# Performance work log

Measured on AMD Instinct MI355X. Metric: run time of the kernel, lower is better.

## Reference

```python
import jax, jax.numpy as jnp
import numpy as np

EPS = 1e-5

def _conv1x1(x, w, b):
    # x: [B,C,H,W], w: [O,C], b: [O] -> [B,O,H,W]
    return jnp.einsum('bchw,oc->bohw', x, w) + b[None, :, None, None]

def setup_inputs() -> dict:
    key = jax.random.key(0)
    ks = jax.random.split(key, 13)
    B, C, H, W = 16, 256, 64, 64
    Ci = C // 2
    s = 0.05
    return {
        'x': jax.random.normal(ks[0], (B, C, H, W), jnp.float32),
        'g_w': jax.random.normal(ks[1], (Ci, C), jnp.float32) * s,
        'g_b': jax.random.normal(ks[2], (Ci,), jnp.float32) * s,
        'theta_w': jax.random.normal(ks[3], (Ci, C), jnp.float32) * s,
        'theta_b': jax.random.normal(ks[4], (Ci,), jnp.float32) * s,
        'phi_w': jax.random.normal(ks[5], (Ci, C), jnp.float32) * s,
        'phi_b': jax.random.normal(ks[6], (Ci,), jnp.float32) * s,
        'w_w': jax.random.normal(ks[7], (C, Ci), jnp.float32) * s,
        'w_b': jax.random.normal(ks[8], (C,), jnp.float32) * s,
        'bn_gamma': jax.random.normal(ks[9], (C,), jnp.float32),
        'bn_beta': jax.random.normal(ks[10], (C,), jnp.float32),
        'bn_mean': jax.random.normal(ks[11], (C,), jnp.float32),
        'bn_var': jax.random.uniform(ks[12], (C,), jnp.float32, 0.5, 1.5),
    }

def reference(x, g_w, g_b, theta_w, theta_b, phi_w, phi_b,
              w_w, w_b, bn_gamma, bn_beta, bn_mean, bn_var):
    B, C, H, W = x.shape
    N = H * W
    Ci = g_w.shape[0]
    # 1x1 conv projections, flatten spatial to N
    g_x = _conv1x1(x, g_w, g_b).reshape(B, Ci, N).transpose(0, 2, 1)        # [B,N,Ci]
    theta_x = _conv1x1(x, theta_w, theta_b).reshape(B, Ci, N).transpose(0, 2, 1)  # [B,N,Ci]
    phi_x = _conv1x1(x, phi_w, phi_b).reshape(B, Ci, N)                     # [B,Ci,N]
    # affinity f = theta @ phi, normalized by N (softmax-free linear attention)
    f_div_C = jnp.einsum('bnc,bcm->bnm', theta_x, phi_x) / N                # [B,N,N]
    y = jnp.einsum('bnm,bmc->bnc', f_div_C, g_x)                            # [B,N,Ci]
    y = y.transpose(0, 2, 1).reshape(B, Ci, H, W)
    # W: 1x1 conv + BatchNorm (eval mode, running stats)
    w_y = _conv1x1(y, w_w, w_b)
    inv = bn_gamma * jax.lax.rsqrt(bn_var + EPS)
    w_y = w_y * inv[None, :, None, None] + (bn_beta - bn_mean * inv)[None, :, None, None]
    return w_y + x
```

## Files before the change

### kernel.cpp

```cpp
#include <hip/hip_runtime.h>
#include <stdint.h>

#define BATCH 16
#define CH    256
#define CI    128
#define NSP   4096
#define KC    4
#define EPSV  1e-5f

typedef unsigned short u16;
typedef __attribute__((ext_vector_type(4))) float f32x4;
typedef __attribute__((ext_vector_type(8))) short bf16x8;

__device__ __forceinline__ u16 f2b(float f) {
  uint32_t u = __float_as_uint(f);
  uint32_t r = u + 0x7FFFu + ((u >> 16) & 1u);
  return (u16)(r >> 16);
}

__device__ __forceinline__ void async16(void* lds, const void* g) {
  __builtin_amdgcn_global_load_lds(
      (const __attribute__((address_space(1))) unsigned int*)g,
      (__attribute__((address_space(3))) unsigned int*)lds, 16, 0, 0);
}

__global__ __launch_bounds__(256) void k_prep2(const float* __restrict__ x,
    u16* __restrict__ xb, float* __restrict__ psum,
    const float* __restrict__ w_w, const float* __restrict__ g_w,
    const float* __restrict__ g_b, const float* __restrict__ theta_w,
    const float* __restrict__ theta_b, const float* __restrict__ phi_w,
    const float* __restrict__ phi_b, const float* __restrict__ w_b,
    const float* __restrict__ bn_g, const float* __restrict__ bn_b,
    const float* __restrict__ bn_m, const float* __restrict__ bn_v,
    float* __restrict__ E, float* __restrict__ KT, float* __restrict__ wg,
    float* __restrict__ tphi, float* __restrict__ q, float* __restrict__ inv,
    float* __restrict__ dconst, float* __restrict__ tb) {
  __shared__ float lbuf[1024];
  const int t = threadIdx.x;
  if (blockIdx.z == BATCH) {
    const int id = blockIdx.y*64 + blockIdx.x;
    if (id < 32) {
      const int o0 = id*8;
      #pragma unroll
      for (int k = 0; k < 4; ++k) { int idx = k*256 + t;
        lbuf[idx] = w_w[(size_t)(o0 + (idx & 7))*CI + (idx >> 3)]; }
      __syncthreads();
      float acc[8] = {0.f};
      for (int j = 0; j < CI; ++j) {
        float gv = g_w[(size_t)j*CH + t];
        #pragma unroll
        for (int r = 0; r < 8; ++r) acc[r] += lbuf[j*8 + r] * gv;
      }
      #pragma unroll
      for (int r = 0; r < 8; ++r) E[(size_t)(o0 + r)*CH + t] = acc[r];
    } else if (id < 64) {
      const int a0 = (id - 32)*8;
      #pragma unroll
      for (int k = 0; k < 4; ++k) { int idx = k*256 + t;
        lbuf[idx] = phi_w[(size_t)(idx >> 3)*CH + a0 + (idx & 7)]; }
      __syncthreads();
      float acc[8] = {0.f};
      for (int i = 0; i < CI; ++i) {
        float tv = theta_w[(size_t)i*CH + t];
        #pragma unroll
        for (int u = 0; u < 8; ++u) acc[u] += lbuf[i*8 + u] * tv;
      }
      #pragma unroll
      for (int u = 0; u < 8; ++u) KT[(size_t)(a0 + u)*CH + t] = acc[u];
    } else if (id == 64) {
      float iv = bn_g[t] * rsqrtf(bn_v[t] + EPSV);
      inv[t] = iv;
      dconst[t] = iv*w_b[t] + bn_b[t] - bn_m[t]*iv;
      float a = 0.f;
      for (int j = 0; j < CI; ++j) a += w_w[(size_t)t*CI + j] * g_b[j];
      wg[t] = a;
      float tp = 0.f, qq = 0.f;
      for (int i = 0; i < CI; ++i) {
        tp += theta_w[(size_t)i*CH + t] * phi_b[i];
        qq += phi_w[(size_t)i*CH + t] * theta_b[i];
      }
      tphi[t] = tp; q[t] = qq;
      lbuf[t] = (t < CI) ? theta_b[t]*phi_b[t] : 0.f;
      __syncthreads();
      for (int s2 = 128; s2 > 0; s2 >>= 1) { if (t < s2) lbuf[t] += lbuf[t + s2]; __syncthreads(); }
      if (t == 0) tb[0] = lbuf[0];
    }
    return;
  }
  const int b = blockIdx.z, c0 = blockIdx.y*64, n0 = blockIdx.x*64;
  const int lane8 = t & 7, rq = t >> 3;
  const float* xp = x + ((size_t)b*CH + c0)*NSP + n0 + lane8*8;
  u16* xbp = xb + ((size_t)b*CH + c0)*NSP + n0 + lane8*8;
  #pragma unroll
  for (int p = 0; p < 2; ++p) {
    const int cl = rq + p*32;
    float4 v0 = *(const float4*)(xp + (size_t)cl*NSP);
    float4 v1 = *(const float4*)(xp + (size_t)cl*NSP + 4);
    float ps = v0.x+v0.y+v0.z+v0.w + v1.x+v1.y+v1.z+v1.w;
    #pragma unroll
    for (int o = 1; o < 8; o <<= 1) ps += __shfl_xor(ps, o, 64);
    if (lane8 == 0) psum[((size_t)b*64 + blockIdx.x)*CH + c0 + cl] = ps;
    bf16x8 bv;
    bv[0]=(short)f2b(v0.x); bv[1]=(short)f2b(v0.y); bv[2]=(short)f2b(v0.z); bv[3]=(short)f2b(v0.w);
    bv[4]=(short)f2b(v1.x); bv[5]=(short)f2b(v1.y); bv[6]=(short)f2b(v1.z); bv[7]=(short)f2b(v1.w);
    *(bf16x8*)(xbp + (size_t)cl*NSP) = bv;
  }
}

__global__ __launch_bounds__(256) void k_tr(const u16* __restrict__ xb, u16* __restrict__ xt) {
  __shared__ u16 tl[64*256];
  const int b = blockIdx.y, n0 = blockIdx.x*64;
  const int t = threadIdx.x;
  const int lane8 = t & 7, rq = t >> 3;
  const u16* src = xb + (size_t)b*CH*NSP + n0;
  #pragma unroll
  for (int p = 0; p < 8; ++p) {
    const int c = rq + p*32;
    bf16x8 v = *(const bf16x8*)(src + (size_t)c*NSP + lane8*8);
    const int cs = c ^ (lane8 << 3);
    #pragma unroll
    for (int j = 0; j < 8; ++j)
      tl[(lane8*8 + j)*256 + cs] = (u16)v[j];
  }
  __syncthreads();
  const int c8 = t & 31, nl = t >> 5;
  u16* dst = xt + ((size_t)b*NSP + n0)*CH;
  #pragma unroll
  for (int p2 = 0; p2 < 8; ++p2) {
    const int n = p2*8 + nl;
    bf16x8 v = *(const bf16x8*)(tl + n*256 + ((c8*8) ^ (p2 << 3)));
    *(bf16x8*)(dst + (size_t)n*CH + c8*8) = v;
  }
}

__global__ __launch_bounds__(256) void k_gram(const u16* __restrict__ xb, float* __restrict__ Sp) {
  __shared__ u16 As[64*64];
  __shared__ u16 Bs[64*64];
  const int TIa[10] = {0,0,0,0,1,1,1,2,2,3};
  const int TJa[10] = {0,1,2,3,1,2,3,2,3,3};
  const int L = blockIdx.x;
  const int wk = (L & 7) * 80 + (L >> 3);
  const int b = wk / 40;
  const int rem = wk % 40;
  const int kc = rem / 10;
  const int tile = rem % 10;
  const int ti = TIa[tile], tj = TJa[tile];
  const int m_base = ti*64, n_base = tj*64;
  const bool diag = (ti == tj);
  const int t = threadIdx.x, wv = t >> 6, l = t & 63;
  const int wr = wv >> 1, wc = wv & 1;
  const int lr = l & 15, lkb = l >> 4;
  const int sr8 = l >> 3, ss = l & 7;
  const u16* xa = xb + (size_t)b*CH*NSP;
  const int kbeg = kc * (NSP/KC);
  f32x4 acc[2][2];
  #pragma unroll
  for (int i = 0; i < 2; ++i)
    #pragma unroll
    for (int j = 0; j < 2; ++j) acc[i][j] = (f32x4){0.f,0.f,0.f,0.f};

  for (int kk = 0; kk < 16; ++kk) {
    const int kpos = kbeg + kk*64;
    #pragma unroll
    for (int j = 0; j < 2; ++j) {
      const int g = wv*2 + j;
      const int r = g*8 + sr8;
      async16(&As[g*512], xa + (size_t)(m_base + r)*NSP + kpos + ((ss ^ (r & 7)) * 8));
    }
    if (!diag) {
      #pragma unroll
      for (int j = 0; j < 2; ++j) {
        const int g = wv*2 + j;
        const int r = g*8 + sr8;
        async16(&Bs[g*512], xa + (size_t)(n_base + r)*NSP + kpos + ((ss ^ (r & 7)) * 8));
      }
    }
    __syncthreads();
    const u16* bsrc = diag ? As : Bs;
    #pragma unroll
    for (int ks = 0; ks < 2; ++ks) {
      bf16x8 A[2], Bf[2];
      #pragma unroll
      for (int mt = 0; mt < 2; ++mt) {
        const int ra = wr*32 + mt*16 + lr;
        A[mt] = *(const bf16x8*)(As + ra*64 + (((ks*4 + lkb) ^ (ra & 7)) * 8));
      }
      #pragma unroll
      for (int nt = 0; nt < 2; ++nt) {
        const int rb = wc*32 + nt*16 + lr;
        Bf[nt] = *(const bf16x8*)(bsrc + rb*64 + (((ks*4 + lkb) ^ (rb & 7)) * 8));
      }
      #pragma unroll
      for (int mt = 0; mt < 2; ++mt)
        #pragma unroll
        for (int nt = 0; nt < 2; ++nt)
          acc[mt][nt] = __builtin_amdgcn_mfma_f32_16x16x32_bf16(A[mt], Bf[nt], acc[mt][nt], 0, 0, 0);
    }
    __syncthreads();
  }
  float* Sb = Sp + (size_t)((b*KC + kc)*10 + tile)*4096;
  const int r0 = (l >> 4) * 4;
  #pragma unroll
  for (int mt = 0; mt < 2; ++mt)
    #pragma unroll
    for (int nt = 0; nt < 2; ++nt)
      #pragma unroll
      for (int rr = 0; rr < 4; ++rr) {
        const int lm = wr*32 + mt*16 + r0 + rr;
        const int lc = wc*32 + nt*16 + lr;
        Sb[lm*64 + lc] = acc[mt][nt][rr];
      }
}

__global__ __launch_bounds__(256) void k_redvec(const float* __restrict__ Sp,
    const float* __restrict__ psum, const float* __restrict__ E,
    const float* __restrict__ KT, const float* __restrict__ q,
    float* __restrict__ S, float* __restrict__ KS, float* __restrict__ Es,
    float* __restrict__ qs) {
  __shared__ float tl[64*65 + 8];
  const int b = blockIdx.y, xx = blockIdx.x, t = threadIdx.x;
  if (xx < 10) {
    const int TIa[10] = {0,0,0,0,1,1,1,2,2,3};
    const int TJa[10] = {0,1,2,3,1,2,3,2,3,3};
    const int ti = TIa[xx], tj = TJa[xx];
    const int row0 = ti*64, col0 = tj*64;
    float* Sb = S + (size_t)b*CH*CH;
    float4 sum[4];
    #pragma unroll
    for (int k = 0; k < 4; ++k) {
      const int slot = t + k*256;
      const int r = slot >> 4, c4 = (slot & 15) * 4;
      float4 s = {0.f,0.f,0.f,0.f};
      #pragma unroll
      for (int kc = 0; kc < KC; ++kc) {
        const float* p = Sp + (size_t)((b*KC + kc)*10 + xx)*4096;
        float4 v = *(const float4*)(p + r*64 + c4);
        s.x += v.x; s.y += v.y; s.z += v.z; s.w += v.w;
      }
      sum[k] = s;
      *(float4*)(Sb + (size_t)(row0 + r)*CH + col0 + c4) = s;
    }
    if (ti != tj) {
      #pragma unroll
      for (int k = 0; k < 4; ++k) {
        const int slot = t + k*256;
        const int r = slot >> 4, c4 = (slot & 15) * 4;
        tl[r*65 + c4+0] = sum[k].x; tl[r*65 + c4+1] = sum[k].y;
        tl[r*65 + c4+2] = sum[k].z; tl[r*65 + c4+3] = sum[k].w;
      }
      __syncthreads();
      #pragma unroll
      for (int k = 0; k < 4; ++k) {
        const int slot = t + k*256;
        const int r = slot >> 4, c4 = (slot & 15) * 4;
        float4 v = { tl[(c4+0)*65 + r], tl[(c4+1)*65 + r],
                     tl[(c4+2)*65 + r], tl[(c4+3)*65 + r] };
        *(float4*)(Sb + (size_t)(col0 + r)*CH + row0 + c4) = v;
      }
    }
  } else {
    float s = 0.f;
    for (int nb = 0; nb < 64; ++nb) s += psum[((size_t)b*64 + nb)*CH + t];
    tl[t] = s;
    __syncthreads();
    float ks = 0.f;
    for (int a = 0; a < CH; ++a) ks += KT[(size_t)a*CH + t] * tl[a];
    KS[(size_t)b*CH + t] = ks;
    float es = 0.f;
    for (int c = 0; c < CH; ++c) es += E[(size_t)t*CH + c] * tl[c];
    Es[(size_t)b*CH + t] = es;
    float p = q[t] * tl[t];
    #pragma unroll
    for (int o = 1; o < 64; o <<= 1) p += __shfl_xor(p, o, 64);
    if ((t & 63) == 0) tl[4160 + (t >> 6)] = p;
    __syncthreads();
    if (t == 0) qs[b] = tl[4160] + tl[4161] + tl[4162] + tl[4163];
  }
}

__global__ __launch_bounds__(256) void k_RP(const float* __restrict__ S,
    const float* __restrict__ E, const float* __restrict__ KT,
    const float* __restrict__ q, const float* __restrict__ KS,
    const float* __restrict__ Es, const float* __restrict__ qs,
    const float* __restrict__ wg, const float* __restrict__ tphi,
    const float* __restrict__ inv, const float* __restrict__ dconst,
    const float* __restrict__ tb, u16* __restrict__ Pb, float* __restrict__ dv) {
  __shared__ float lEt[2048];
  __shared__ float lRt[2048];
  __shared__ float red[32];
  const int b = blockIdx.y, o0 = blockIdx.x*8, t = threadIdx.x;
  #pragma unroll
  for (int k = 0; k < 8; ++k) { int idx = k*256 + t;
    lEt[idx] = E[(size_t)(o0 + (idx & 7))*CH + (idx >> 3)]; }
  __syncthreads();
  const float* Sb = S + (size_t)b*CH*CH;
  float acc[8] = {0.f};
  for (int c = 0; c < CH; ++c) {
    float sv = Sb[(size_t)c*CH + t];
    #pragma unroll
    for (int r = 0; r < 8; ++r) acc[r] += lEt[c*8 + r] * sv;
  }
  #pragma unroll
  for (int r = 0; r < 8; ++r) lRt[t*8 + r] = acc[r];
  const float qt = q[t];
  #pragma unroll
  for (int r = 0; r < 8; ++r) {
    float p = acc[r] * qt;
    #pragma unroll
    for (int o = 1; o < 64; o <<= 1) p += __shfl_xor(p, o, 64);
    if ((t & 63) == 0) red[r*4 + (t >> 6)] = p;
  }
  __syncthreads();
  float acc2[8] = {0.f};
  for (int a = 0; a < CH; ++a) {
    float kv = KT[(size_t)a*CH + t];
    #pragma unroll
    for (int r = 0; r < 8; ++r) acc2[r] += lRt[a*8 + r] * kv;
  }
  const float ksv = KS[(size_t)b*CH + t], tpv = tphi[t];
  u16* Pbb = Pb + (size_t)b*CH*CH;
  #pragma unroll
  for (int r = 0; r < 8; ++r) {
    int o = o0 + r;
    float val = (acc2[r] + wg[o]*ksv + (Es[(size_t)b*CH + o] + (float)NSP*wg[o])*tpv)
                * inv[o] * (1.f/(float)NSP);
    if (o == t) val += 1.f;
    Pbb[(size_t)o*CH + t] = f2b(val);
  }
  if (t < 8) {
    int o = o0 + t;
    float iv = inv[o], wgo = wg[o], tb0 = tb[0];
    float rq = red[t*4] + red[t*4+1] + red[t*4+2] + red[t*4+3];
    float t2 = rq + wgo*qs[b] + Es[(size_t)b*CH + o]*tb0;
    dv[(size_t)b*CH + o] = iv*(t2*(1.f/(float)NSP) + wgo*tb0) + dconst[o];
  }
}

__global__ __launch_bounds__(512, 4) void k_apply(const u16* __restrict__ Pb,
    const u16* __restrict__ xt, const float* __restrict__ dv,
    float* __restrict__ out) {
  __shared__ union {
    u16   bx[64*256];
    float fe[8][16][68];
  } sm;
  const int b = blockIdx.y, n0 = blockIdx.x*64;
  const int t = threadIdx.x, w = t >> 6, l = t & 63;
  {
    const u16* src = xt + ((size_t)b*NSP + n0)*CH;
    const int r = t >> 3, sbase = t & 7;
    #pragma unroll
    for (int it = 0; it < 4; ++it) {
      int slot = sbase + it*8;
      bf16x8 v = *(const bf16x8*)(src + (size_t)r*CH + slot*8);
      *(bf16x8*)(sm.bx + r*256 + ((slot ^ (r & 7)) * 8)) = v;
    }
  }
  __syncthreads();
  const int m0 = w*32;
  const int lr = l & 15, lkb = l >> 4;
  const int sw = lr & 7;
  const u16* Pp = Pb + (size_t)b*CH*CH;
  f32x4 acc[2][4];
  #pragma unroll
  for (int i = 0; i < 2; ++i)
    #pragma unroll
    for (int j = 0; j < 4; ++j) acc[i][j] = (f32x4){0.f,0.f,0.f,0.f};
  #pragma unroll
  for (int kk = 0; kk < 8; ++kk) {
    bf16x8 A[2], Bf[4];
    #pragma unroll
    for (int mt = 0; mt < 2; ++mt)
      A[mt] = *(const bf16x8*)(Pp + (size_t)(m0 + mt*16 + lr)*CH + kk*32 + lkb*8);
    #pragma unroll
    for (int nt = 0; nt < 4; ++nt) {
      int slot = kk*4 + lkb;
      Bf[nt] = *(const bf16x8*)(sm.bx + (nt*16 + lr)*256 + ((slot ^ sw) * 8));
    }
    #pragma unroll
    for (int mt = 0; mt < 2; ++mt)
      #pragma unroll
      for (int nt = 0; nt < 4; ++nt)
        acc[mt][nt] = __builtin_amdgcn_mfma_f32_16x16x32_bf16(A[mt], Bf[nt], acc[mt][nt], 0, 0, 0);
  }
  __syncthreads();
  float* ob = out + (size_t)b*CH*NSP;
  const int r0 = (l >> 4) * 4;
  #pragma unroll
  for (int mt = 0; mt < 2; ++mt) {
    #pragma unroll
    for (int rr = 0; rr < 4; ++rr) {
      float dval = dv[(size_t)b*CH + m0 + mt*16 + r0 + rr];
      #pragma unroll
      for (int nt = 0; nt < 4; ++nt)
        sm.fe[w][r0 + rr][nt*16 + lr] = acc[mt][nt][rr] + dval;
    }
    #pragma unroll
    for (int i = 0; i < 4; ++i) {
      int s = l + 64*i;
      int rrow = s >> 4, c4 = (s & 15) * 4;
      float4 v = *(const float4*)&sm.fe[w][rrow][c4];
      *(float4*)&ob[(size_t)(m0 + mt*16 + rrow)*NSP + n0 + c4] = v;
    }
  }
}

static constexpr size_t XT_OFF = 0;
static constexpr size_t S_OFF  = 33554432;
static constexpr size_t PB_OFF = 37748736;
static constexpr size_t PS_OFF = 39845888;
static constexpr size_t E_OFF  = 40894464;
static constexpr size_t KT_OFF = 41156608;
static constexpr size_t WG_OFF = 41418752;
static constexpr size_t TP_OFF = 41419776;
static constexpr size_t QV_OFF = 41420800;
static constexpr size_t IV_OFF = 41421824;
static constexpr size_t DC_OFF = 41422848;
static constexpr size_t TB_OFF = 41423872;
static constexpr size_t KS_OFF = 41424896;
static constexpr size_t ES_OFF = 41441280;
static constexpr size_t QS_OFF = 41457664;
static constexpr size_t DV_OFF = 41458688;

extern "C" void kernel_launch(void* const* d_in, const int* in_sizes, int n_in,
                              void* d_out, int out_size, void* d_ws, size_t ws_size,
                              hipStream_t stream) {
  const float* x       = (const float*)d_in[0];
  const float* g_w     = (const float*)d_in[1];
  const float* g_b     = (const float*)d_in[2];
  const float* theta_w = (const float*)d_in[3];
  const float* theta_b = (const float*)d_in[4];
  const float* phi_w   = (const float*)d_in[5];
  const float* phi_b   = (const float*)d_in[6];
  const float* w_w     = (const float*)d_in[7];
  const float* w_b     = (const float*)d_in[8];
  const float* bn_g    = (const float*)d_in[9];
  const float* bn_b    = (const float*)d_in[10];
  const float* bn_m    = (const float*)d_in[11];
  const float* bn_v    = (const float*)d_in[12];
  float* out = (float*)d_out;
  char* ws = (char*)d_ws;
  u16*   XT = (u16*)(ws + XT_OFF);
  float* S  = (float*)(ws + S_OFF);
  u16*   Pb = (u16*)(ws + PB_OFF);
  float* PS = (float*)(ws + PS_OFF);
  float* E  = (float*)(ws + E_OFF);
  float* KT = (float*)(ws + KT_OFF);
  float* WG = (float*)(ws + WG_OFF);
  float* TP = (float*)(ws + TP_OFF);
  float* QV = (float*)(ws + QV_OFF);
  float* IV = (float*)(ws + IV_OFF);
  float* DC = (float*)(ws + DC_OFF);
  float* TB = (float*)(ws + TB_OFF);
  float* KS = (float*)(ws + KS_OFF);
  float* ES = (float*)(ws + ES_OFF);
  float* QS = (float*)(ws + QS_OFF);
  float* DV = (float*)(ws + DV_OFF);
  u16*   Xb = (u16*)d_out;
  float* Sp = (float*)((char*)d_out + 33554432);

  k_prep2 <<<dim3(64, 4, BATCH+1),        256, 0, stream>>>(x, Xb, PS,
            w_w, g_w, g_b, theta_w, theta_b, phi_w, phi_b, w_b, bn_g, bn_b, bn_m, bn_v,
            E, KT, WG, TP, QV, IV, DC, TB);
  k_gram  <<<dim3(640),                   256, 0, stream>>>(Xb, Sp);
  k_tr    <<<dim3(64, BATCH),             256, 0, stream>>>(Xb, XT);
  k_redvec<<<dim3(11, BATCH),             256, 0, stream>>>(Sp, PS, E, KT, QV, S, KS, ES, QS);
  k_RP    <<<dim3(32, BATCH),             256, 0, stream>>>(S, E, KT, QV, KS, ES, QS, WG, TP, IV, DC, TB, Pb, DV);
  k_apply <<<dim3(NSP/64, BATCH),         512, 0, stream>>>(Pb, XT, DV, out);
}
```

Measured before the change: 128.9 us.

## Fuse bf16 transpose into prep kernel and drop separate transpose launch

The prep kernel now gives each block a 64-position slab across all 256 channels. It converts x to bf16 and writes both the channel-major copy and, through an LDS tile, the transposed position-major copy. This removes the k_tr launch and its re-read of the bf16 buffer from global memory. In exchange the grid shrinks to 65x17 blocks, each doing more serial loads and using a 32 KB LDS union, which may lower occupancy and latency hiding.

```diff
diff --git a/kernel.cpp b/kernel.cpp
--- a/kernel.cpp
+++ b/kernel.cpp
@@ -24,8 +24,8 @@
       (__attribute__((address_space(3))) unsigned int*)lds, 16, 0, 0);
 }
 
-__global__ __launch_bounds__(256) void k_prep2(const float* __restrict__ x,
-    u16* __restrict__ xb, float* __restrict__ psum,
+__global__ __launch_bounds__(256) void k_prep(const float* __restrict__ x,
+    u16* __restrict__ xb, u16* __restrict__ xt, float* __restrict__ psum,
     const float* __restrict__ w_w, const float* __restrict__ g_w,
     const float* __restrict__ g_b, const float* __restrict__ theta_w,
     const float* __restrict__ theta_b, const float* __restrict__ phi_w,
@@ -35,10 +35,11 @@
     float* __restrict__ E, float* __restrict__ KT, float* __restrict__ wg,
     float* __restrict__ tphi, float* __restrict__ q, float* __restrict__ inv,
     float* __restrict__ dconst, float* __restrict__ tb) {
-  __shared__ float lbuf[1024];
+  __shared__ union { u16 tl[64*256]; float lbuf[1024]; } sm;
   const int t = threadIdx.x;
   if (blockIdx.z == BATCH) {
-    const int id = blockIdx.y*64 + blockIdx.x;
+    float* lbuf = sm.lbuf;
+    const int id = blockIdx.x;
     if (id < 32) {
       const int o0 = id*8;
       #pragma unroll
@@ -87,40 +88,28 @@
     }
     return;
   }
-  const int b = blockIdx.z, c0 = blockIdx.y*64, n0 = blockIdx.x*64;
+  if (blockIdx.x >= 64) return;
+  const int b = blockIdx.z, n0 = blockIdx.x*64;
   const int lane8 = t & 7, rq = t >> 3;
-  const float* xp = x + ((size_t)b*CH + c0)*NSP + n0 + lane8*8;
-  u16* xbp = xb + ((size_t)b*CH + c0)*NSP + n0 + lane8*8;
-  #pragma unroll
-  for (int p = 0; p < 2; ++p) {
-    const int cl = rq + p*32;
-    float4 v0 = *(const float4*)(xp + (size_t)cl*NSP);
-    float4 v1 = *(const float4*)(xp + (size_t)cl*NSP + 4);
+  const float* xp = x + (size_t)b*CH*NSP + n0 + lane8*8;
+  u16* xbp = xb + (size_t)b*CH*NSP + n0 + lane8*8;
+  #pragma unroll
+  for (int p = 0; p < 8; ++p) {
+    const int c = rq + p*32;
+    float4 v0 = *(const float4*)(xp + (size_t)c*NSP);
+    float4 v1 = *(const float4*)(xp + (size_t)c*NSP + 4);
     float ps = v0.x+v0.y+v0.z+v0.w + v1.x+v1.y+v1.z+v1.w;
     #pragma unroll
     for (int o = 1; o < 8; o <<= 1) ps += __shfl_xor(ps, o, 64);
-    if (lane8 == 0) psum[((size_t)b*64 + blockIdx.x)*CH + c0 + cl] = ps;
+    if (lane8 == 0) psum[((size_t)b*64 + blockIdx.x)*CH + c] = ps;
     bf16x8 bv;
     bv[0]=(short)f2b(v0.x); bv[1]=(short)f2b(v0.y); bv[2]=(short)f2b(v0.z); bv[3]=(short)f2b(v0.w);
     bv[4]=(short)f2b(v1.x); bv[5]=(short)f2b(v1.y); bv[6]=(short)f2b(v1.z); bv[7]=(short)f2b(v1.w);
-    *(bf16x8*)(xbp + (size_t)cl*NSP) = bv;
-  }
-}
-
-__global__ __launch_bounds__(256) void k_tr(const u16* __restrict__ xb, u16* __restrict__ xt) {
-  __shared__ u16 tl[64*256];
-  const int b = blockIdx.y, n0 = blockIdx.x*64;
-  const int t = threadIdx.x;
-  const int lane8 = t & 7, rq = t >> 3;
-  const u16* src = xb + (size_t)b*CH*NSP + n0;
-  #pragma unroll
-  for (int p = 0; p < 8; ++p) {
-    const int c = rq + p*32;
-    bf16x8 v = *(const bf16x8*)(src + (size_t)c*NSP + lane8*8);
+    *(bf16x8*)(xbp + (size_t)c*NSP) = bv;
     const int cs = c ^ (lane8 << 3);
     #pragma unroll
     for (int j = 0; j < 8; ++j)
-      tl[(lane8*8 + j)*256 + cs] = (u16)v[j];
+      sm.tl[(lane8*8 + j)*256 + cs] = (u16)bv[j];
   }
   __syncthreads();
   const int c8 = t & 31, nl = t >> 5;
@@ -128,7 +117,7 @@
   #pragma unroll
   for (int p2 = 0; p2 < 8; ++p2) {
     const int n = p2*8 + nl;
-    bf16x8 v = *(const bf16x8*)(tl + n*256 + ((c8*8) ^ (p2 << 3)));
+    bf16x8 v = *(const bf16x8*)(sm.tl + n*256 + ((c8*8) ^ (p2 << 3)));
     *(bf16x8*)(dst + (size_t)n*CH + c8*8) = v;
   }
 }
@@ -458,11 +447,10 @@
   u16*   Xb = (u16*)d_out;
   float* Sp = (float*)((char*)d_out + 33554432);
 
-  k_prep2 <<<dim3(64, 4, BATCH+1),        256, 0, stream>>>(x, Xb, PS,
+  k_prep  <<<dim3(65, 1, BATCH+1),        256, 0, stream>>>(x, Xb, XT, PS,
             w_w, g_w, g_b, theta_w, theta_b, phi_w, phi_b, w_b, bn_g, bn_b, bn_m, bn_v,
             E, KT, WG, TP, QV, IV, DC, TB);
   k_gram  <<<dim3(640),                   256, 0, stream>>>(Xb, Sp);
-  k_tr    <<<dim3(64, BATCH),             256, 0, stream>>>(Xb, XT);
   k_redvec<<<dim3(11, BATCH),             256, 0, stream>>>(Sp, PS, E, KT, QV, S, KS, ES, QS);
   k_RP    <<<dim3(32, BATCH),             256, 0, stream>>>(S, E, KT, QV, KS, ES, QS, WG, TP, IV, DC, TB, Pb, DV);
   k_apply <<<dim3(NSP/64, BATCH),         512, 0, stream>>>(Pb, XT, DV, out);
```

New measurement: 120.2 us. 6.8% less time.

## Fuse bf16 transpose into apply kernel and drop separate transpose pass

Applied to the files above, without the earlier changes.

Removes the standalone k_tr kernel, which wrote a transposed bf16 copy of x to workspace. k_apply now reads the channel-major bf16 x directly and transposes it into LDS with a new XOR swizzle, and the MFMA B-fragment reads use a matching swizzle. Xb moves from the output buffer into workspace so k_apply can still read it after output writes begin. This saves one launch and a full read/write of the 32 MB bf16 tensor, but each apply block now does scattered 2-byte LDS stores with possible bank conflicts and strided global reads.

```diff
diff --git a/kernel.cpp b/kernel.cpp
--- a/kernel.cpp
+++ b/kernel.cpp
@@ -24,7 +24,7 @@
       (__attribute__((address_space(3))) unsigned int*)lds, 16, 0, 0);
 }
 
-__global__ __launch_bounds__(256) void k_prep2(const float* __restrict__ x,
+__global__ __launch_bounds__(256) void k_prep(const float* __restrict__ x,
     u16* __restrict__ xb, float* __restrict__ psum,
     const float* __restrict__ w_w, const float* __restrict__ g_w,
     const float* __restrict__ g_b, const float* __restrict__ theta_w,
@@ -104,32 +104,6 @@
     bv[0]=(short)f2b(v0.x); bv[1]=(short)f2b(v0.y); bv[2]=(short)f2b(v0.z); bv[3]=(short)f2b(v0.w);
     bv[4]=(short)f2b(v1.x); bv[5]=(short)f2b(v1.y); bv[6]=(short)f2b(v1.z); bv[7]=(short)f2b(v1.w);
     *(bf16x8*)(xbp + (size_t)cl*NSP) = bv;
-  }
-}
-
-__global__ __launch_bounds__(256) void k_tr(const u16* __restrict__ xb, u16* __restrict__ xt) {
-  __shared__ u16 tl[64*256];
-  const int b = blockIdx.y, n0 = blockIdx.x*64;
-  const int t = threadIdx.x;
-  const int lane8 = t & 7, rq = t >> 3;
-  const u16* src = xb + (size_t)b*CH*NSP + n0;
-  #pragma unroll
-  for (int p = 0; p < 8; ++p) {
-    const int c = rq + p*32;
-    bf16x8 v = *(const bf16x8*)(src + (size_t)c*NSP + lane8*8);
-    const int cs = c ^ (lane8 << 3);
-    #pragma unroll
-    for (int j = 0; j < 8; ++j)
-      tl[(lane8*8 + j)*256 + cs] = (u16)v[j];
-  }
-  __syncthreads();
-  const int c8 = t & 31, nl = t >> 5;
-  u16* dst = xt + ((size_t)b*NSP + n0)*CH;
-  #pragma unroll
-  for (int p2 = 0; p2 < 8; ++p2) {
-    const int n = p2*8 + nl;
-    bf16x8 v = *(const bf16x8*)(tl + n*256 + ((c8*8) ^ (p2 << 3)));
-    *(bf16x8*)(dst + (size_t)n*CH + c8*8) = v;
   }
 }
 
@@ -337,28 +311,31 @@
 }
 
 __global__ __launch_bounds__(512, 4) void k_apply(const u16* __restrict__ Pb,
-    const u16* __restrict__ xt, const float* __restrict__ dv,
+    const u16* __restrict__ xb, const float* __restrict__ dv,
     float* __restrict__ out) {
   __shared__ union {
-    u16   bx[64*256];
+    u16   tl[64*256];
     float fe[8][16][68];
   } sm;
   const int b = blockIdx.y, n0 = blockIdx.x*64;
   const int t = threadIdx.x, w = t >> 6, l = t & 63;
   {
-    const u16* src = xt + ((size_t)b*NSP + n0)*CH;
-    const int r = t >> 3, sbase = t & 7;
-    #pragma unroll
-    for (int it = 0; it < 4; ++it) {
-      int slot = sbase + it*8;
-      bf16x8 v = *(const bf16x8*)(src + (size_t)r*CH + slot*8);
-      *(bf16x8*)(sm.bx + r*256 + ((slot ^ (r & 7)) * 8)) = v;
+    const u16* src = xb + (size_t)b*CH*NSP + n0;
+    const int lane8 = t & 7, rq = t >> 3;
+    #pragma unroll
+    for (int p = 0; p < 4; ++p) {
+      const int c = rq + p*64;
+      bf16x8 v = *(const bf16x8*)(src + (size_t)c*NSP + lane8*8);
+      #pragma unroll
+      for (int j = 0; j < 8; ++j) {
+        const int K = j ^ lane8;
+        sm.tl[(lane8*8 + j)*256 + (c ^ (K << 3))] = (u16)v[j];
+      }
     }
   }
   __syncthreads();
   const int m0 = w*32;
   const int lr = l & 15, lkb = l >> 4;
-  const int sw = lr & 7;
   const u16* Pp = Pb + (size_t)b*CH*CH;
   f32x4 acc[2][4];
   #pragma unroll
@@ -373,8 +350,10 @@
       A[mt] = *(const bf16x8*)(Pp + (size_t)(m0 + mt*16 + lr)*CH + kk*32 + lkb*8);
     #pragma unroll
     for (int nt = 0; nt < 4; ++nt) {
-      int slot = kk*4 + lkb;
-      Bf[nt] = *(const bf16x8*)(sm.bx + (nt*16 + lr)*256 + ((slot ^ sw) * 8));
+      const int row = nt*16 + lr;
+      const int K = (row & 7) ^ (row >> 3);
+      const int slot = kk*4 + lkb;
+      Bf[nt] = *(const bf16x8*)(sm.tl + row*256 + ((slot ^ K) * 8));
     }
     #pragma unroll
     for (int mt = 0; mt < 2; ++mt)
@@ -404,7 +383,7 @@
   }
 }
 
-static constexpr size_t XT_OFF = 0;
+static constexpr size_t XB_OFF = 0;
 static constexpr size_t S_OFF  = 33554432;
 static constexpr size_t PB_OFF = 37748736;
 static constexpr size_t PS_OFF = 39845888;
@@ -439,7 +418,7 @@
   const float* bn_v    = (const float*)d_in[12];
   float* out = (float*)d_out;
   char* ws = (char*)d_ws;
-  u16*   XT = (u16*)(ws + XT_OFF);
+  u16*   Xb = (u16*)(ws + XB_OFF);
   float* S  = (float*)(ws + S_OFF);
   u16*   Pb = (u16*)(ws + PB_OFF);
   float* PS = (float*)(ws + PS_OFF);
@@ -455,15 +434,13 @@
   float* ES = (float*)(ws + ES_OFF);
   float* QS = (float*)(ws + QS_OFF);
   float* DV = (float*)(ws + DV_OFF);
-  u16*   Xb = (u16*)d_out;
   float* Sp = (float*)((char*)d_out + 33554432);
 
-  k_prep2 <<<dim3(64, 4, BATCH+1),        256, 0, stream>>>(x, Xb, PS,
+  k_prep  <<<dim3(64, 4, BATCH+1),        256, 0, stream>>>(x, Xb, PS,
             w_w, g_w, g_b, theta_w, theta_b, phi_w, phi_b, w_b, bn_g, bn_b, bn_m, bn_v,
             E, KT, WG, TP, QV, IV, DC, TB);
   k_gram  <<<dim3(640),                   256, 0, stream>>>(Xb, Sp);
-  k_tr    <<<dim3(64, BATCH),             256, 0, stream>>>(Xb, XT);
   k_redvec<<<dim3(11, BATCH),             256, 0, stream>>>(Sp, PS, E, KT, QV, S, KS, ES, QS);
   k_RP    <<<dim3(32, BATCH),             256, 0, stream>>>(S, E, KT, QV, KS, ES, QS, WG, TP, IV, DC, TB, Pb, DV);
-  k_apply <<<dim3(NSP/64, BATCH),         512, 0, stream>>>(Pb, XT, DV, out);
-}
+  k_apply <<<dim3(NSP/64, BATCH),         512, 0, stream>>>(Pb, Xb, DV, out);
+}
```

Measured after the change: 118.0 us. 1.09x faster.
